# Performance work log

Hardware: AMD Instinct MI355X
Metric: run time of the kernel (lower is better)

The kernel has to match this reference:

```python
import jax, jax.numpy as jnp
import numpy as np

N_NODES = 200000
N_EDGES = 6400000


def _gcn_layer(x, W, b, src, dst, n):
    # PyG GCNConv: add self loops, sym-normalize, propagate src->dst, add bias.
    loop = jnp.arange(n, dtype=src.dtype)
    s = jnp.concatenate([src, loop])
    d = jnp.concatenate([dst, loop])
    deg = jax.ops.segment_sum(jnp.ones_like(s, dtype=x.dtype), d, num_segments=n)
    dinv = jnp.where(deg > 0, jax.lax.rsqrt(deg), 0.0)
    norm = dinv[s] * dinv[d]                      # [E+N]
    h = x @ W                                     # [N, F_out]
    msg = h[s] * norm[:, None]                    # gather + scale
    out = jax.ops.segment_sum(msg, d, num_segments=n)  # scatter-add
    return out + b


def setup_inputs() -> dict:
    key = jax.random.key(0)
    ks = jax.random.split(key, 4)
    x = jax.random.normal(ks[0], (N_NODES, 3), dtype=jnp.float32)
    edge_index = jax.random.randint(ks[1], (2, N_EDGES), 0, N_NODES, dtype=jnp.int64 if jax.config.read('jax_enable_x64') else jnp.int32)
    W1 = jax.random.normal(ks[2], (3, 16), dtype=jnp.float32) * (1.0 / np.sqrt(3.0))
    b1 = jnp.zeros((16,), dtype=jnp.float32)
    W2 = jax.random.normal(ks[3], (16, 3), dtype=jnp.float32) * (1.0 / np.sqrt(16.0))
    b2 = jnp.zeros((3,), dtype=jnp.float32)
    return {"x": x, "edge_index": edge_index, "W1": W1, "b1": b1, "W2": W2, "b2": b2}


def reference(x, edge_index, W1, b1, W2, b2):
    src, dst = edge_index[0], edge_index[1]
    n = x.shape[0]
    h = _gcn_layer(x, W1, b1, src, dst, n)
    h = jax.nn.relu(h)
    out = _gcn_layer(h, W2, b2, src, dst, n)
    return out
```

## Files before the change

kernel.cpp:

```cpp
#include <hip/hip_runtime.h>

#define NN 200000
#define NE 6400000
#define NB 800
#define NWA 256
#define CHUNK 25000
#define CHUNK4 6250
#define BUFCAP 44
#define CAPB 8704
#define OVF 256

#define OFF_E    0
#define OFF_C    6963200
#define OFF_RP   6964000
#define OFF_DG   7164000
#define OFF_DINV 7364000
#define OFF_XS   7564000
#define OFF_HS2  8364000

__global__ void __launch_bounds__(1024) k_scatter(const int* __restrict__ src,
                                                  const int* __restrict__ dst,
                                                  int* __restrict__ C,
                                                  int* __restrict__ E) {
    __shared__ int wbase[NB];
    __shared__ int cnt[NB];
    __shared__ int buf[NB * BUFCAP];
    __shared__ int ovf[2 * OVF];
    __shared__ int ovfn;
    int w = blockIdx.x, t = threadIdx.x;
    for (int b = t; b < NB; b += 1024) cnt[b] = 0;
    if (t == 0) ovfn = 0;
    __syncthreads();
    int lo = w * CHUNK;
    const int4* src4 = (const int4*)(src + lo);
    const int4* dst4 = (const int4*)(dst + lo);
    for (int i = t; i < CHUNK4; i += 1024) {
        int4 s4 = src4[i];
        int4 d4 = dst4[i];
#pragma unroll
        for (int q = 0; q < 4; ++q) {
            int s = (&s4.x)[q], d = (&d4.x)[q];
            int b = d >> 8;
            int rec = s | ((d & 255) << 18);
            int pos = atomicAdd(&cnt[b], 1);
            if (pos < BUFCAP) buf[b * BUFCAP + pos] = rec;
            else {
                int o = atomicAdd(&ovfn, 1);
                ovf[2 * o] = rec;
                ovf[2 * o + 1] = (b << 16) | pos;
            }
        }
    }
    __syncthreads();
    for (int b = t; b < NB; b += 1024)
        wbase[b] = b * CAPB + atomicAdd(&C[b], cnt[b]);
    __syncthreads();
    for (int idx = t; idx < NB * BUFCAP; idx += 1024) {
        int b = idx / BUFCAP, j = idx - b * BUFCAP;
        int c = cnt[b];
        if (j < (c < BUFCAP ? c : BUFCAP)) E[wbase[b] + j] = buf[idx];
    }
    for (int o = t; o < ovfn; o += 1024) {
        int rec = ovf[2 * o], bp = ovf[2 * o + 1];
        E[wbase[bp >> 16] + (bp & 0xFFFF)] = rec;
    }
}

__global__ void __launch_bounds__(512) k_sort(const float* __restrict__ x, int* __restrict__ E,
                       const int* __restrict__ C,
                       int* __restrict__ RP, int* __restrict__ DG,
                       float* __restrict__ dinv, float4* __restrict__ xs4) {
    __shared__ int stg[CAPB];
    __shared__ int cnt[256];
    __shared__ int pos[256];
    int b = blockIdx.x, t = threadIdx.x;
    int lo = b * CAPB;
    int n = C[b];
    int n4 = n >> 2;
    if (t < 256) cnt[t] = 0;
    __syncthreads();
    const int4* E4 = (const int4*)(E + lo);
    for (int i = t; i < n4; i += 512) {
        int4 r = E4[i];
        ((int4*)stg)[i] = r;
        atomicAdd(&cnt[((unsigned)r.x) >> 18], 1);
        atomicAdd(&cnt[((unsigned)r.y) >> 18], 1);
        atomicAdd(&cnt[((unsigned)r.z) >> 18], 1);
        atomicAdd(&cnt[((unsigned)r.w) >> 18], 1);
    }
    for (int i = (n4 << 2) + t; i < n; i += 512) {
        int r = E[lo + i];
        stg[i] = r;
        atomicAdd(&cnt[((unsigned)r) >> 18], 1);
    }
    __syncthreads();
    if (t < 256) pos[t] = cnt[t];
    __syncthreads();
    for (int off = 1; off < 256; off <<= 1) {
        int v = 0;
        if (t < 256 && t >= off) v = pos[t - off];
        __syncthreads();
        if (t < 256) pos[t] += v;
        __syncthreads();
    }
    if (t < 256) {
        int c = cnt[t];
        int excl = pos[t] - c;
        int node = (b << 8) + t;
        if (node < NN) {
            RP[node] = lo + excl;
            DG[node] = c;
            float di = rsqrtf(1.0f + (float)c);
            dinv[node] = di;
            xs4[node] = make_float4(x[3 * node] * di, x[3 * node + 1] * di,
                                    x[3 * node + 2] * di, 0.f);
        }
        cnt[t] = excl;
    }
    __syncthreads();
    for (int i = t; i < n4; i += 512) {
        int4 r = ((const int4*)stg)[i];
#pragma unroll
        for (int q = 0; q < 4; ++q) {
            int rec = (&r.x)[q];
            int slot = atomicAdd(&cnt[((unsigned)rec) >> 18], 1);
            E[lo + slot] = rec & 0x3FFFF;
        }
    }
    for (int i = (n4 << 2) + t; i < n; i += 512) {
        int rec = stg[i];
        int slot = atomicAdd(&cnt[((unsigned)rec) >> 18], 1);
        E[lo + slot] = rec & 0x3FFFF;
    }
}

__global__ void k_gather1(const int* __restrict__ E, const int* __restrict__ RP,
                          const int* __restrict__ DG, const float* __restrict__ dinv,
                          const float4* __restrict__ xs4, const float* __restrict__ W1,
                          const float* __restrict__ b1, const float* __restrict__ W2,
                          float4* __restrict__ hs24) {
    int t = threadIdx.x;
    int seg = t >> 4, lane = t & 15;
    int n = blockIdx.x * 16 + seg;
    int rp = RP[n], dg = DG[n];
    float s0 = 0.f, s1 = 0.f, s2 = 0.f;
    for (int j = lane; j < dg; j += 16) {
        float4 m = xs4[E[rp + j]];
        s0 += m.x; s1 += m.y; s2 += m.z;
    }
#pragma unroll
    for (int msk = 1; msk < 16; msk <<= 1) {
        s0 += __shfl_xor(s0, msk, 16);
        s1 += __shfl_xor(s1, msk, 16);
        s2 += __shfl_xor(s2, msk, 16);
    }
    float di = dinv[n];
    float4 self = xs4[n];
    float a0 = di * (s0 + self.x);
    float a1 = di * (s1 + self.y);
    float a2 = di * (s2 + self.z);
    int k = lane;
    float v = a0 * W1[k] + a1 * W1[16 + k] + a2 * W1[32 + k] + b1[k];
    v = v > 0.f ? v : 0.f;
    float o0 = v * W2[3 * k + 0];
    float o1 = v * W2[3 * k + 1];
    float o2 = v * W2[3 * k + 2];
#pragma unroll
    for (int msk = 1; msk < 16; msk <<= 1) {
        o0 += __shfl_xor(o0, msk, 16);
        o1 += __shfl_xor(o1, msk, 16);
        o2 += __shfl_xor(o2, msk, 16);
    }
    if (lane == 0)
        hs24[n] = make_float4(o0 * di, o1 * di, o2 * di, 0.f);
}

__global__ void k_gather2(const int* __restrict__ E, const int* __restrict__ RP,
                          const int* __restrict__ DG, const float* __restrict__ dinv,
                          const float4* __restrict__ hs24, const float* __restrict__ b2,
                          float* __restrict__ out) {
    __shared__ float smo[48];
    int t = threadIdx.x;
    int seg = t >> 4, lane = t & 15;
    int n = blockIdx.x * 16 + seg;
    int rp = RP[n], dg = DG[n];
    float s0 = 0.f, s1 = 0.f, s2 = 0.f;
    for (int j = lane; j < dg; j += 16) {
        float4 m = hs24[E[rp + j]];
        s0 += m.x; s1 += m.y; s2 += m.z;
    }
#pragma unroll
    for (int msk = 1; msk < 16; msk <<= 1) {
        s0 += __shfl_xor(s0, msk, 16);
        s1 += __shfl_xor(s1, msk, 16);
        s2 += __shfl_xor(s2, msk, 16);
    }
    if (lane == 0) {
        float di = dinv[n];
        float4 self = hs24[n];
        smo[seg * 3 + 0] = di * (s0 + self.x) + b2[0];
        smo[seg * 3 + 1] = di * (s1 + self.y) + b2[1];
        smo[seg * 3 + 2] = di * (s2 + self.z) + b2[2];
    }
    __syncthreads();
    if (t < 48) out[(size_t)blockIdx.x * 48 + t] = smo[t];
}

extern "C" void kernel_launch(void* const* d_in, const int* in_sizes, int n_in,
                              void* d_out, int out_size, void* d_ws, size_t ws_size,
                              hipStream_t stream) {
    const float* x  = (const float*)d_in[0];
    const int* ei   = (const int*)d_in[1];
    const float* W1 = (const float*)d_in[2];
    const float* b1 = (const float*)d_in[3];
    const float* W2 = (const float*)d_in[4];
    const float* b2 = (const float*)d_in[5];
    const int* src = ei;
    const int* dst = ei + NE;
    float* ws = (float*)d_ws;
    int* wsi = (int*)d_ws;
    float* out = (float*)d_out;

    int* E      = wsi + OFF_E;
    int* C      = wsi + OFF_C;
    int* RP     = wsi + OFF_RP;
    int* DG     = wsi + OFF_DG;
    float* dinv = ws + OFF_DINV;
    float4* xs4 = (float4*)(ws + OFF_XS);
    float4* hs24 = (float4*)(ws + OFF_HS2);

    hipMemsetAsync(C, 0, NB * sizeof(int), stream);
    k_scatter<<<NWA, 1024, 0, stream>>>(src, dst, C, E);
    k_sort<<<NB, 512, 0, stream>>>(x, E, C, RP, DG, dinv, xs4);
    k_gather1<<<NN / 16, 256, 0, stream>>>(E, RP, DG, dinv, xs4, W1, b1, W2, hs24);
    k_gather2<<<NN / 16, 256, 0, stream>>>(E, RP, DG, dinv, hs24, b2, out);
}
```

Baseline: 221.9 us.

## Pack row pointer/degree, fold dinv into float4 w, use 32 lanes per node

Row pointer and degree are packed into a single int2 array, and dinv is stored in the unused w slot of the xs4/hs24 float4s, so each node needs fewer separate metadata loads. The gather kernels now assign 32 lanes per destination node instead of 16, with 8 nodes per block. Since the average degree is about 32, each lane typically does one gather. The wider groups trade more idle lanes on low-degree nodes and twice as many blocks for less looping and fewer metadata reads.

```diff
diff --git a/kernel.cpp b/kernel.cpp
--- a/kernel.cpp
+++ b/kernel.cpp
@@ -13,7 +13,6 @@
 #define OFF_E    0
 #define OFF_C    6963200
 #define OFF_RP   6964000
-#define OFF_DG   7164000
 #define OFF_DINV 7364000
 #define OFF_XS   7564000
 #define OFF_HS2  8364000
@@ -68,8 +67,8 @@
 
 __global__ void __launch_bounds__(512) k_sort(const float* __restrict__ x, int* __restrict__ E,
                        const int* __restrict__ C,
-                       int* __restrict__ RP, int* __restrict__ DG,
-                       float* __restrict__ dinv, float4* __restrict__ xs4) {
+                       int2* __restrict__ RD,
+                       float4* __restrict__ xs4) {
     __shared__ int stg[CAPB];
     __shared__ int cnt[256];
     __shared__ int pos[256];
@@ -108,12 +107,10 @@
         int excl = pos[t] - c;
         int node = (b << 8) + t;
         if (node < NN) {
-            RP[node] = lo + excl;
-            DG[node] = c;
+            RD[node] = make_int2(lo + excl, c);
             float di = rsqrtf(1.0f + (float)c);
-            dinv[node] = di;
             xs4[node] = make_float4(x[3 * node] * di, x[3 * node + 1] * di,
-                                    x[3 * node + 2] * di, 0.f);
+                                    x[3 * node + 2] * di, di);
         }
         cnt[t] = excl;
     }
@@ -134,32 +131,36 @@
     }
 }
 
-__global__ void k_gather1(const int* __restrict__ E, const int* __restrict__ RP,
-                          const int* __restrict__ DG, const float* __restrict__ dinv,
+__global__ void k_gather1(const int* __restrict__ E, const int2* __restrict__ RD,
                           const float4* __restrict__ xs4, const float* __restrict__ W1,
                           const float* __restrict__ b1, const float* __restrict__ W2,
                           float4* __restrict__ hs24) {
     int t = threadIdx.x;
-    int seg = t >> 4, lane = t & 15;
-    int n = blockIdx.x * 16 + seg;
-    int rp = RP[n], dg = DG[n];
+    int seg = t >> 5, lane = t & 31;
+    int n = blockIdx.x * 8 + seg;
+    int2 rd = RD[n];
+    int rp = rd.x, dg = rd.y;
     float s0 = 0.f, s1 = 0.f, s2 = 0.f;
-    for (int j = lane; j < dg; j += 16) {
+    if (lane < dg) {
+        float4 m = xs4[E[rp + lane]];
+        s0 = m.x; s1 = m.y; s2 = m.z;
+    }
+    for (int j = lane + 32; j < dg; j += 32) {
         float4 m = xs4[E[rp + j]];
         s0 += m.x; s1 += m.y; s2 += m.z;
     }
 #pragma unroll
-    for (int msk = 1; msk < 16; msk <<= 1) {
-        s0 += __shfl_xor(s0, msk, 16);
-        s1 += __shfl_xor(s1, msk, 16);
-        s2 += __shfl_xor(s2, msk, 16);
-    }
-    float di = dinv[n];
+    for (int msk = 1; msk < 32; msk <<= 1) {
+        s0 += __shfl_xor(s0, msk, 32);
+        s1 += __shfl_xor(s1, msk, 32);
+        s2 += __shfl_xor(s2, msk, 32);
+    }
     float4 self = xs4[n];
+    float di = self.w;
     float a0 = di * (s0 + self.x);
     float a1 = di * (s1 + self.y);
     float a2 = di * (s2 + self.z);
-    int k = lane;
+    int k = lane & 15;
     float v = a0 * W1[k] + a1 * W1[16 + k] + a2 * W1[32 + k] + b1[k];
     v = v > 0.f ? v : 0.f;
     float o0 = v * W2[3 * k + 0];
@@ -172,38 +173,42 @@
         o2 += __shfl_xor(o2, msk, 16);
     }
     if (lane == 0)
-        hs24[n] = make_float4(o0 * di, o1 * di, o2 * di, 0.f);
-}
-
-__global__ void k_gather2(const int* __restrict__ E, const int* __restrict__ RP,
-                          const int* __restrict__ DG, const float* __restrict__ dinv,
+        hs24[n] = make_float4(o0 * di, o1 * di, o2 * di, di);
+}
+
+__global__ void k_gather2(const int* __restrict__ E, const int2* __restrict__ RD,
                           const float4* __restrict__ hs24, const float* __restrict__ b2,
                           float* __restrict__ out) {
-    __shared__ float smo[48];
+    __shared__ float smo[24];
     int t = threadIdx.x;
-    int seg = t >> 4, lane = t & 15;
-    int n = blockIdx.x * 16 + seg;
-    int rp = RP[n], dg = DG[n];
+    int seg = t >> 5, lane = t & 31;
+    int n = blockIdx.x * 8 + seg;
+    int2 rd = RD[n];
+    int rp = rd.x, dg = rd.y;
     float s0 = 0.f, s1 = 0.f, s2 = 0.f;
-    for (int j = lane; j < dg; j += 16) {
+    if (lane < dg) {
+        float4 m = hs24[E[rp + lane]];
+        s0 = m.x; s1 = m.y; s2 = m.z;
+    }
+    for (int j = lane + 32; j < dg; j += 32) {
         float4 m = hs24[E[rp + j]];
         s0 += m.x; s1 += m.y; s2 += m.z;
     }
 #pragma unroll
-    for (int msk = 1; msk < 16; msk <<= 1) {
-        s0 += __shfl_xor(s0, msk, 16);
-        s1 += __shfl_xor(s1, msk, 16);
-        s2 += __shfl_xor(s2, msk, 16);
+    for (int msk = 1; msk < 32; msk <<= 1) {
+        s0 += __shfl_xor(s0, msk, 32);
+        s1 += __shfl_xor(s1, msk, 32);
+        s2 += __shfl_xor(s2, msk, 32);
     }
     if (lane == 0) {
-        float di = dinv[n];
         float4 self = hs24[n];
+        float di = self.w;
         smo[seg * 3 + 0] = di * (s0 + self.x) + b2[0];
         smo[seg * 3 + 1] = di * (s1 + self.y) + b2[1];
         smo[seg * 3 + 2] = di * (s2 + self.z) + b2[2];
     }
     __syncthreads();
-    if (t < 48) out[(size_t)blockIdx.x * 48 + t] = smo[t];
+    if (t < 24) out[(size_t)blockIdx.x * 24 + t] = smo[t];
 }
 
 extern "C" void kernel_launch(void* const* d_in, const int* in_sizes, int n_in,
@@ -223,15 +228,13 @@
 
     int* E      = wsi + OFF_E;
     int* C      = wsi + OFF_C;
-    int* RP     = wsi + OFF_RP;
-    int* DG     = wsi + OFF_DG;
-    float* dinv = ws + OFF_DINV;
+    int2* RD    = (int2*)(wsi + OFF_RP);
     float4* xs4 = (float4*)(ws + OFF_XS);
     float4* hs24 = (float4*)(ws + OFF_HS2);
 
     hipMemsetAsync(C, 0, NB * sizeof(int), stream);
     k_scatter<<<NWA, 1024, 0, stream>>>(src, dst, C, E);
-    k_sort<<<NB, 512, 0, stream>>>(x, E, C, RP, DG, dinv, xs4);
-    k_gather1<<<NN / 16, 256, 0, stream>>>(E, RP, DG, dinv, xs4, W1, b1, W2, hs24);
-    k_gather2<<<NN / 16, 256, 0, stream>>>(E, RP, DG, dinv, hs24, b2, out);
-}
+    k_sort<<<NB, 512, 0, stream>>>(x, E, C, RD, xs4);
+    k_gather1<<<NN / 8, 256, 0, stream>>>(E, RD, xs4, W1, b1, W2, hs24);
+    k_gather2<<<NN / 8, 256, 0, stream>>>(E, RD, hs24, b2, out);
+}
```

Measured after the change: 227.7 us. 1.03x slower.

## Pack row pointer/degree, fold dinv into float4, prefetch four edges per lane

Applied to the files above, without the earlier changes.

Row pointer and degree are now written as a single int2, and dinv is stored in the unused w lane of the xs4/hs24 float4s, so separate dinv/DG arrays and their loads go away. Both gather kernels issue four clamped edge-index loads and four feature gathers up front, masking out-of-range ones, before falling back to the loop for degrees over 64. The goal is more memory-level parallelism for the typical ~33-edge rows and fewer dependent loads, at the cost of redundant loads for short rows and more registers.

```diff
diff --git a/kernel.cpp b/kernel.cpp
--- a/kernel.cpp
+++ b/kernel.cpp
@@ -13,8 +13,6 @@
 #define OFF_E    0
 #define OFF_C    6963200
 #define OFF_RP   6964000
-#define OFF_DG   7164000
-#define OFF_DINV 7364000
 #define OFF_XS   7564000
 #define OFF_HS2  8364000
 
@@ -68,8 +66,8 @@
 
 __global__ void __launch_bounds__(512) k_sort(const float* __restrict__ x, int* __restrict__ E,
                        const int* __restrict__ C,
-                       int* __restrict__ RP, int* __restrict__ DG,
-                       float* __restrict__ dinv, float4* __restrict__ xs4) {
+                       int2* __restrict__ RD,
+                       float4* __restrict__ xs4) {
     __shared__ int stg[CAPB];
     __shared__ int cnt[256];
     __shared__ int pos[256];
@@ -108,12 +106,10 @@
         int excl = pos[t] - c;
         int node = (b << 8) + t;
         if (node < NN) {
-            RP[node] = lo + excl;
-            DG[node] = c;
+            RD[node] = make_int2(lo + excl, c);
             float di = rsqrtf(1.0f + (float)c);
-            dinv[node] = di;
             xs4[node] = make_float4(x[3 * node] * di, x[3 * node + 1] * di,
-                                    x[3 * node + 2] * di, 0.f);
+                                    x[3 * node + 2] * di, di);
         }
         cnt[t] = excl;
     }
@@ -134,17 +130,33 @@
     }
 }
 
-__global__ void k_gather1(const int* __restrict__ E, const int* __restrict__ RP,
-                          const int* __restrict__ DG, const float* __restrict__ dinv,
+__global__ void k_gather1(const int* __restrict__ E, const int2* __restrict__ RD,
                           const float4* __restrict__ xs4, const float* __restrict__ W1,
                           const float* __restrict__ b1, const float* __restrict__ W2,
                           float4* __restrict__ hs24) {
     int t = threadIdx.x;
     int seg = t >> 4, lane = t & 15;
     int n = blockIdx.x * 16 + seg;
-    int rp = RP[n], dg = DG[n];
-    float s0 = 0.f, s1 = 0.f, s2 = 0.f;
-    for (int j = lane; j < dg; j += 16) {
+    int2 rd = RD[n];
+    int rp = rd.x, dg = rd.y;
+    int last = rp + (dg > 0 ? dg - 1 : 0);
+    int j0 = rp + lane;
+    int e0 = E[j0 < last ? j0 : last];
+    int e1 = E[j0 + 16 < last ? j0 + 16 : last];
+    int e2 = E[j0 + 32 < last ? j0 + 32 : last];
+    int e3 = E[j0 + 48 < last ? j0 + 48 : last];
+    float4 m0 = xs4[e0];
+    float4 m1 = xs4[e1];
+    float4 m2 = xs4[e2];
+    float4 m3 = xs4[e3];
+    float f0 = (lane      < dg) ? 1.f : 0.f;
+    float f1 = (lane + 16 < dg) ? 1.f : 0.f;
+    float f2 = (lane + 32 < dg) ? 1.f : 0.f;
+    float f3 = (lane + 48 < dg) ? 1.f : 0.f;
+    float s0 = f0 * m0.x + f1 * m1.x + f2 * m2.x + f3 * m3.x;
+    float s1 = f0 * m0.y + f1 * m1.y + f2 * m2.y + f3 * m3.y;
+    float s2 = f0 * m0.z + f1 * m1.z + f2 * m2.z + f3 * m3.z;
+    for (int j = lane + 64; j < dg; j += 16) {
         float4 m = xs4[E[rp + j]];
         s0 += m.x; s1 += m.y; s2 += m.z;
     }
@@ -154,8 +166,8 @@
         s1 += __shfl_xor(s1, msk, 16);
         s2 += __shfl_xor(s2, msk, 16);
     }
-    float di = dinv[n];
     float4 self = xs4[n];
+    float di = self.w;
     float a0 = di * (s0 + self.x);
     float a1 = di * (s1 + self.y);
     float a2 = di * (s2 + self.z);
@@ -172,20 +184,36 @@
         o2 += __shfl_xor(o2, msk, 16);
     }
     if (lane == 0)
-        hs24[n] = make_float4(o0 * di, o1 * di, o2 * di, 0.f);
-}
-
-__global__ void k_gather2(const int* __restrict__ E, const int* __restrict__ RP,
-                          const int* __restrict__ DG, const float* __restrict__ dinv,
+        hs24[n] = make_float4(o0 * di, o1 * di, o2 * di, di);
+}
+
+__global__ void k_gather2(const int* __restrict__ E, const int2* __restrict__ RD,
                           const float4* __restrict__ hs24, const float* __restrict__ b2,
                           float* __restrict__ out) {
     __shared__ float smo[48];
     int t = threadIdx.x;
     int seg = t >> 4, lane = t & 15;
     int n = blockIdx.x * 16 + seg;
-    int rp = RP[n], dg = DG[n];
-    float s0 = 0.f, s1 = 0.f, s2 = 0.f;
-    for (int j = lane; j < dg; j += 16) {
+    int2 rd = RD[n];
+    int rp = rd.x, dg = rd.y;
+    int last = rp + (dg > 0 ? dg - 1 : 0);
+    int j0 = rp + lane;
+    int e0 = E[j0 < last ? j0 : last];
+    int e1 = E[j0 + 16 < last ? j0 + 16 : last];
+    int e2 = E[j0 + 32 < last ? j0 + 32 : last];
+    int e3 = E[j0 + 48 < last ? j0 + 48 : last];
+    float4 m0 = hs24[e0];
+    float4 m1 = hs24[e1];
+    float4 m2 = hs24[e2];
+    float4 m3 = hs24[e3];
+    float f0 = (lane      < dg) ? 1.f : 0.f;
+    float f1 = (lane + 16 < dg) ? 1.f : 0.f;
+    float f2 = (lane + 32 < dg) ? 1.f : 0.f;
+    float f3 = (lane + 48 < dg) ? 1.f : 0.f;
+    float s0 = f0 * m0.x + f1 * m1.x + f2 * m2.x + f3 * m3.x;
+    float s1 = f0 * m0.y + f1 * m1.y + f2 * m2.y + f3 * m3.y;
+    float s2 = f0 * m0.z + f1 * m1.z + f2 * m2.z + f3 * m3.z;
+    for (int j = lane + 64; j < dg; j += 16) {
         float4 m = hs24[E[rp + j]];
         s0 += m.x; s1 += m.y; s2 += m.z;
     }
@@ -196,8 +224,8 @@
         s2 += __shfl_xor(s2, msk, 16);
     }
     if (lane == 0) {
-        float di = dinv[n];
         float4 self = hs24[n];
+        float di = self.w;
         smo[seg * 3 + 0] = di * (s0 + self.x) + b2[0];
         smo[seg * 3 + 1] = di * (s1 + self.y) + b2[1];
         smo[seg * 3 + 2] = di * (s2 + self.z) + b2[2];
@@ -223,15 +251,13 @@
 
     int* E      = wsi + OFF_E;
     int* C      = wsi + OFF_C;
-    int* RP     = wsi + OFF_RP;
-    int* DG     = wsi + OFF_DG;
-    float* dinv = ws + OFF_DINV;
+    int2* RD    = (int2*)(wsi + OFF_RP);
     float4* xs4 = (float4*)(ws + OFF_XS);
     float4* hs24 = (float4*)(ws + OFF_HS2);
 
     hipMemsetAsync(C, 0, NB * sizeof(int), stream);
     k_scatter<<<NWA, 1024, 0, stream>>>(src, dst, C, E);
-    k_sort<<<NB, 512, 0, stream>>>(x, E, C, RP, DG, dinv, xs4);
-    k_gather1<<<NN / 16, 256, 0, stream>>>(E, RP, DG, dinv, xs4, W1, b1, W2, hs24);
-    k_gather2<<<NN / 16, 256, 0, stream>>>(E, RP, DG, dinv, hs24, b2, out);
-}
+    k_sort<<<NB, 512, 0, stream>>>(x, E, C, RD, xs4);
+    k_gather1<<<NN / 16, 256, 0, stream>>>(E, RD, xs4, W1, b1, W2, hs24);
+    k_gather2<<<NN / 16, 256, 0, stream>>>(E, RD, hs24, b2, out);
+}
```

New measurement: 212.7 us. -4.1%, faster.
